# Kernel tuning notes

Measured on AMD Instinct MI355X. Metric: run time of the kernel, lower is better.

## Reference

```python
import jax, jax.numpy as jnp
import numpy as np

B, L, D = 64, 2048, 60
P, PS = 16, 30  # num patches, patch size

def setup_inputs() -> dict:
    key = jax.random.key(0)
    k1, k2, k3, k4 = jax.random.split(key, 4)
    seq1M = jax.random.normal(k1, (B, L, D), dtype=jnp.float32)
    seq2M = jax.random.normal(k2, (B, L, D), dtype=jnp.float32)
    geo = jax.random.normal(k3, (B, P, PS, PS), dtype=jnp.float32)
    patches = jax.random.randint(k4, (B, P, 2), 0, L - PS, dtype=jnp.int32)
    return {"seq1M": seq1M, "seq2M": seq2M, "geo": geo, "patches": patches}

def reference(seq1M, seq2M, geo, patches):
    # rows: seq1M[b, patches[b,p,0] : +PS, :] -> [B,P,PS,D]
    # cols: seq2M[b, patches[b,p,1] : +PS, :] -> [B,P,PS,D]
    offs = jnp.arange(PS)  # [PS]
    bidx = jnp.arange(seq1M.shape[0])[:, None, None]  # [B,1,1]
    ridx = patches[:, :, 0][..., None] + offs  # [B,P,PS]
    cidx = patches[:, :, 1][..., None] + offs  # [B,P,PS]
    rows = seq1M[bidx, ridx]  # [B,P,PS,D]
    cols = seq2M[bidx, cidx]  # [B,P,PS,D]
    # block[b,p,a,c] = concat(rows[b,p,c], cols[b,p,a], geo[b,p,a,c])
    shp = rows.shape[:2] + (PS, PS, rows.shape[-1])  # [B,P,PS,PS,D]
    row_t = jnp.broadcast_to(rows[:, :, None, :, :], shp)
    col_t = jnp.broadcast_to(cols[:, :, :, None, :], shp)
    return jnp.concatenate([row_t, col_t, geo[..., None]], axis=-1)  # [B,P,PS,PS,2D+1]
```

## Files before the change

kernel.cpp:

```cpp
#include <hip/hip_runtime.h>


constexpr int B_    = 64;
constexpr int L_    = 2048;
constexpr int D_    = 60;
constexpr int P_    = 16;
constexpr int PS_   = 30;
constexpr int KOUT  = 2 * D_ + 1;
constexpr int NPAIR = PS_ * PS_;
constexpr int CHUNK = NPAIR * KOUT;
constexpr int ROWF  = PS_ * KOUT;
constexpr int AP_F4 = 2 * ROWF / 4;
constexpr int NAP   = PS_ / 2;

constexpr int NT = 512;
constexpr int NS = (AP_F4 + NT - 1) / NT;

constexpr int RPAD  = 64;
constexpr int CBASE = PS_ * RPAD;
constexpr int GBASE = 2 * CBASE;
constexpr int LDSF  = GBASE + PS_ * 32;

__device__ __forceinline__ int perm60(int k) { return (k & 3) * 15 + (k >> 2); }

__global__ __launch_bounds__(NT) void make_blocks_38860864094557_kernel(
    const float* __restrict__ seq1, const float* __restrict__ seq2,
    const float* __restrict__ geo,  const int* __restrict__ patches,
    float* __restrict__ out)
{
    __shared__ float sh[LDSF];

    const int bp  = blockIdx.x;
    const int b   = bp / P_;
    const int tid = threadIdx.x;

    const int r0 = patches[bp * 2 + 0];
    const int c0 = patches[bp * 2 + 1];

    const float* s1 = seq1 + ((size_t)b * L_ + r0) * D_;
    const float* s2 = seq2 + ((size_t)b * L_ + c0) * D_;
    const float* gg = geo  + (size_t)bp * NPAIR;

    for (int i = tid; i < PS_ * D_; i += NT) {
        const int c = i / D_;
        const int k = i - c * D_;
        const int pa = c * RPAD + perm60(k);
        sh[pa]         = s1[i];
        sh[CBASE + pa] = s2[i];
    }
    for (int i = tid; i < NPAIR; i += NT) {
        const int a = i / PS_;
        const int c = i - a * PS_;
        sh[GBASE + a * 32 + c] = gg[i];
    }
    __syncthreads();

    int offb[NS][4];
    int strb[NS][4];
    bool valid[NS];
#pragma unroll
    for (int s = 0; s < NS; ++s) {
        const int u4 = tid + s * NT;
        valid[s] = (u4 < AP_F4);
        const int u4c = valid[s] ? u4 : (AP_F4 - 1);
#pragma unroll
        for (int j = 0; j < 4; ++j) {
            const int u  = 4 * u4c + j;
            const int ah = (u >= ROWF) ? 1 : 0;
            const int r  = u - ah * ROWF;
            const int c  = r / KOUT;
            const int k  = r - c * KOUT;
            int off, st;
            if (k < D_)          { off = c * RPAD + perm60(k);                st = 0;         }
            else if (k < 2*D_)   { off = CBASE + ah * RPAD + perm60(k - D_);  st = 2 * RPAD;  }
            else                 { off = GBASE + ah * 32 + c;                 st = 2 * 32;    }
            offb[s][j] = off * 4;
            strb[s][j] = st * 4;
        }
    }

    float4* outf4 = reinterpret_cast<float4*>(out + (size_t)bp * CHUNK);
    const char* shb = reinterpret_cast<const char*>(sh);

    for (int ap = 0; ap < NAP; ++ap) {
#pragma unroll
        for (int s = 0; s < NS; ++s) {
            if (valid[s]) {
                float4 v;
                v.x = *reinterpret_cast<const float*>(shb + offb[s][0]);
                v.y = *reinterpret_cast<const float*>(shb + offb[s][1]);
                v.z = *reinterpret_cast<const float*>(shb + offb[s][2]);
                v.w = *reinterpret_cast<const float*>(shb + offb[s][3]);
                outf4[ap * AP_F4 + tid + s * NT] = v;
            }
#pragma unroll
            for (int j = 0; j < 4; ++j) offb[s][j] += strb[s][j];
        }
    }
}

extern "C" void kernel_launch(void* const* d_in, const int* in_sizes, int n_in,
                              void* d_out, int out_size, void* d_ws, size_t ws_size,
                              hipStream_t stream) {
    const float* seq1    = (const float*)d_in[0];
    const float* seq2    = (const float*)d_in[1];
    const float* geo     = (const float*)d_in[2];
    const int*   patches = (const int*)d_in[3];
    float*       out     = (float*)d_out;

    const int grid = B_ * P_;
    make_blocks_38860864094557_kernel<<<grid, NT, 0, stream>>>(seq1, seq2, geo, patches, out);
}
```

Before: 113.0 us.

## Process four patches per block with double-buffered LDS and XCD-aware chunk mapping

Each 1024-thread block now handles four consecutive (b,p) chunks. It prefetches the next chunk's global data into registers while sweeping the current one out of a double-buffered shared array. Block indices are remapped so that chunks assigned to one XCD are contiguous. This is meant to hide global load latency behind the output stores and to amortise setup work. The cost is only 256 blocks at one block per CU, which lowers occupancy for a store-bound kernel.

```diff
diff --git a/kernel.cpp b/kernel.cpp
--- a/kernel.cpp
+++ b/kernel.cpp
@@ -13,50 +13,115 @@
 constexpr int AP_F4 = 2 * ROWF / 4;
 constexpr int NAP   = PS_ / 2;
 
-constexpr int NT = 512;
-constexpr int NS = (AP_F4 + NT - 1) / NT;
+constexpr int NT  = 1024;
+constexpr int NS  = 2;
+constexpr int CPB = 4;
+constexpr int NBLK = (B_ * P_) / CPB;
+constexpr int XCDS = 8;
+constexpr int CH_PER_XCD = (B_ * P_) / XCDS;
 
 constexpr int RPAD  = 64;
 constexpr int CBASE = PS_ * RPAD;
 constexpr int GBASE = 2 * CBASE;
 constexpr int LDSF  = GBASE + PS_ * 32;
 
+constexpr int NSRC = 2 * PS_ * D_ + NPAIR;
+constexpr int NSTG = (NSRC + NT - 1) / NT;
+
 __device__ __forceinline__ int perm60(int k) { return (k & 3) * 15 + (k >> 2); }
 
-__global__ __launch_bounds__(NT) void make_blocks_38860864094557_kernel(
+__device__ __forceinline__ int stage_lds_off(int i) {
+    if (i < PS_ * D_)     { int c = i / D_, k = i - c * D_; return c * RPAD + perm60(k); }
+    if (i < 2 * PS_ * D_) { int j = i - PS_ * D_; int c = j / D_, k = j - c * D_;
+                            return CBASE + c * RPAD + perm60(k); }
+    int j = i - 2 * PS_ * D_; int a = j / PS_, c = j - a * PS_;
+    return GBASE + a * 32 + c;
+}
+
+__device__ __forceinline__ void issue_loads(const float* __restrict__ seq1,
+                                            const float* __restrict__ seq2,
+                                            const float* __restrict__ geo,
+                                            int bp, int r0, int c0, int tid,
+                                            float stg[NSTG]) {
+    const float* s1 = seq1 + ((size_t)(bp / P_) * L_ + r0) * D_;
+    const float* s2 = seq2 + ((size_t)(bp / P_) * L_ + c0) * D_;
+    const float* gg = geo  + (size_t)bp * NPAIR;
+#pragma unroll
+    for (int n = 0; n < NSTG; ++n) {
+        const int i = tid + n * NT;
+        if (i < NSRC) {
+            float v;
+            if (i < PS_ * D_)          v = s1[i];
+            else if (i < 2 * PS_ * D_) v = s2[i - PS_ * D_];
+            else                       v = gg[i - 2 * PS_ * D_];
+            stg[n] = v;
+        }
+    }
+}
+
+__device__ __forceinline__ void write_lds(float* __restrict__ buf, const float stg[NSTG],
+                                          const int loff[NSTG], int tid) {
+#pragma unroll
+    for (int n = 0; n < NSTG; ++n) {
+        if (tid + n * NT < NSRC) buf[loff[n]] = stg[n];
+    }
+}
+
+__device__ __forceinline__ void sweep(const char* __restrict__ shb,
+                                      const int off0[NS][4], const int strb[NS][4],
+                                      const bool valid[NS],
+                                      float4* __restrict__ outf4, int tid) {
+    int offb[NS][4];
+#pragma unroll
+    for (int s = 0; s < NS; ++s)
+#pragma unroll
+        for (int j = 0; j < 4; ++j) offb[s][j] = off0[s][j];
+
+    for (int ap = 0; ap < NAP; ++ap) {
+#pragma unroll
+        for (int s = 0; s < NS; ++s) {
+            if (valid[s]) {
+                float4 v;
+                v.x = *reinterpret_cast<const float*>(shb + offb[s][0]);
+                v.y = *reinterpret_cast<const float*>(shb + offb[s][1]);
+                v.z = *reinterpret_cast<const float*>(shb + offb[s][2]);
+                v.w = *reinterpret_cast<const float*>(shb + offb[s][3]);
+                outf4[(size_t)ap * AP_F4 + tid + s * NT] = v;
+            }
+#pragma unroll
+            for (int j = 0; j < 4; ++j) offb[s][j] += strb[s][j];
+        }
+    }
+}
+
+__global__ __launch_bounds__(NT, 1) void make_blocks_38860864094557_kernel(
     const float* __restrict__ seq1, const float* __restrict__ seq2,
     const float* __restrict__ geo,  const int* __restrict__ patches,
     float* __restrict__ out)
 {
-    __shared__ float sh[LDSF];
+    __shared__ float sh[2][LDSF];
 
-    const int bp  = blockIdx.x;
-    const int b   = bp / P_;
     const int tid = threadIdx.x;
+    const int bid = blockIdx.x;
+    const int xcd = bid & (XCDS - 1);
+    const int sub = bid >> 3;
+    const int bp0 = xcd * CH_PER_XCD + sub * CPB;
 
-    const int r0 = patches[bp * 2 + 0];
-    const int c0 = patches[bp * 2 + 1];
+    int r0s[CPB], c0s[CPB];
+#pragma unroll
+    for (int t = 0; t < CPB; ++t) {
+        r0s[t] = patches[(bp0 + t) * 2 + 0];
+        c0s[t] = patches[(bp0 + t) * 2 + 1];
+    }
 
-    const float* s1 = seq1 + ((size_t)b * L_ + r0) * D_;
-    const float* s2 = seq2 + ((size_t)b * L_ + c0) * D_;
-    const float* gg = geo  + (size_t)bp * NPAIR;
+    int loff[NSTG];
+#pragma unroll
+    for (int n = 0; n < NSTG; ++n) {
+        const int i = tid + n * NT;
+        loff[n] = (i < NSRC) ? stage_lds_off(i) : 0;
+    }
 
-    for (int i = tid; i < PS_ * D_; i += NT) {
-        const int c = i / D_;
-        const int k = i - c * D_;
-        const int pa = c * RPAD + perm60(k);
-        sh[pa]         = s1[i];
-        sh[CBASE + pa] = s2[i];
-    }
-    for (int i = tid; i < NPAIR; i += NT) {
-        const int a = i / PS_;
-        const int c = i - a * PS_;
-        sh[GBASE + a * 32 + c] = gg[i];
-    }
-    __syncthreads();
-
-    int offb[NS][4];
-    int strb[NS][4];
+    int off0[NS][4], strb[NS][4];
     bool valid[NS];
 #pragma unroll
     for (int s = 0; s < NS; ++s) {
@@ -71,32 +136,41 @@
             const int c  = r / KOUT;
             const int k  = r - c * KOUT;
             int off, st;
-            if (k < D_)          { off = c * RPAD + perm60(k);                st = 0;         }
-            else if (k < 2*D_)   { off = CBASE + ah * RPAD + perm60(k - D_);  st = 2 * RPAD;  }
-            else                 { off = GBASE + ah * 32 + c;                 st = 2 * 32;    }
-            offb[s][j] = off * 4;
+            if (k < D_)          { off = c * RPAD + perm60(k);                st = 0;        }
+            else if (k < 2*D_)   { off = CBASE + ah * RPAD + perm60(k - D_);  st = 2 * RPAD; }
+            else                 { off = GBASE + ah * 32 + c;                 st = 2 * 32;   }
+            off0[s][j] = off * 4;
             strb[s][j] = st * 4;
         }
     }
 
-    float4* outf4 = reinterpret_cast<float4*>(out + (size_t)bp * CHUNK);
-    const char* shb = reinterpret_cast<const char*>(sh);
+    float4* o0 = reinterpret_cast<float4*>(out + (size_t)(bp0 + 0) * CHUNK);
+    float4* o1 = reinterpret_cast<float4*>(out + (size_t)(bp0 + 1) * CHUNK);
+    float4* o2 = reinterpret_cast<float4*>(out + (size_t)(bp0 + 2) * CHUNK);
+    float4* o3 = reinterpret_cast<float4*>(out + (size_t)(bp0 + 3) * CHUNK);
 
-    for (int ap = 0; ap < NAP; ++ap) {
-#pragma unroll
-        for (int s = 0; s < NS; ++s) {
-            if (valid[s]) {
-                float4 v;
-                v.x = *reinterpret_cast<const float*>(shb + offb[s][0]);
-                v.y = *reinterpret_cast<const float*>(shb + offb[s][1]);
-                v.z = *reinterpret_cast<const float*>(shb + offb[s][2]);
-                v.w = *reinterpret_cast<const float*>(shb + offb[s][3]);
-                outf4[ap * AP_F4 + tid + s * NT] = v;
-            }
-#pragma unroll
-            for (int j = 0; j < 4; ++j) offb[s][j] += strb[s][j];
-        }
-    }
+    float stg[NSTG];
+
+    issue_loads(seq1, seq2, geo, bp0 + 0, r0s[0], c0s[0], tid, stg);
+    write_lds(sh[0], stg, loff, tid);
+    __syncthreads();
+
+    issue_loads(seq1, seq2, geo, bp0 + 1, r0s[1], c0s[1], tid, stg);
+    sweep(reinterpret_cast<const char*>(sh[0]), off0, strb, valid, o0, tid);
+    write_lds(sh[1], stg, loff, tid);
+    __syncthreads();
+
+    issue_loads(seq1, seq2, geo, bp0 + 2, r0s[2], c0s[2], tid, stg);
+    sweep(reinterpret_cast<const char*>(sh[1]), off0, strb, valid, o1, tid);
+    write_lds(sh[0], stg, loff, tid);
+    __syncthreads();
+
+    issue_loads(seq1, seq2, geo, bp0 + 3, r0s[3], c0s[3], tid, stg);
+    sweep(reinterpret_cast<const char*>(sh[0]), off0, strb, valid, o2, tid);
+    write_lds(sh[1], stg, loff, tid);
+    __syncthreads();
+
+    sweep(reinterpret_cast<const char*>(sh[1]), off0, strb, valid, o3, tid);
 }
 
 extern "C" void kernel_launch(void* const* d_in, const int* in_sizes, int n_in,
@@ -108,6 +182,5 @@
     const int*   patches = (const int*)d_in[3];
     float*       out     = (float*)d_out;
 
-    const int grid = B_ * P_;
-    make_blocks_38860864094557_kernel<<<grid, NT, 0, stream>>>(seq1, seq2, geo, patches, out);
+    make_blocks_38860864094557_kernel<<<NBLK, NT, 0, stream>>>(seq1, seq2, geo, patches, out);
 }
```

Measured after the change: 115.0 us. About the same (+1.8%).
